# Kernel optimization log

Measured on AMD Instinct MI355X. Metric: run time of the kernel, lower is better.

## Reference

```python
import jax, jax.numpy as jnp
import numpy as np

NUM_EXPERT = 16
IN_FEAT = 1024
OUT_FEAT = 2048
N_TOKENS = 4096


def setup_inputs() -> dict:
    key = jax.random.key(0)
    k1, k2, k3 = jax.random.split(key, 3)
    x = jax.random.uniform(k1, (N_TOKENS, IN_FEAT), dtype=jnp.float32)
    gate = jax.random.randint(k2, (N_TOKENS,), 0, NUM_EXPERT, dtype=jnp.int32)
    # expert weights: [num_expert, out_feat, in_feat]
    weight = jax.random.normal(k3, (NUM_EXPERT, OUT_FEAT, IN_FEAT), dtype=jnp.float32) * 0.02
    return {"x": x, "gate": gate, "weight": weight}


def reference(x, gate, weight):
    # out[b] = weight[gate[b]] @ x[b]
    # Avoid materializing weight[gate] ([B, O, I] would be huge): scan over the
    # small, fixed expert axis with input masking (tokens not routed to expert e
    # contribute zero rows to that expert's GEMM).
    B = x.shape[0]
    E, O, I = weight.shape
    out0 = jnp.zeros((B, O), dtype=x.dtype)

    def body(out, ew):
        e, W = ew  # W: [O, I]
        xm = jnp.where((gate == e)[:, None], x, 0.0)  # [B, I] masked tokens
        return out + jnp.einsum("bi,oi->bo", xm, W), None

    out, _ = jax.lax.scan(body, out0, (jnp.arange(E), weight))
    return out
```

## Files before the change

kernel.cpp:

```cpp
#include <hip/hip_runtime.h>
#include <hip/hip_bf16.h>
#include <stdint.h>

#define N_TOKENS   4096
#define IN_FEAT    1024
#define OUT_FEAT   2048
#define NUM_EXPERT 16

#define BM 256
#define BN 128
#define BK 32
#define NT (IN_FEAT / BK)
#define MAX_TILES 32
#define MAX_ROWS  8192

typedef __bf16 bf16x8 __attribute__((ext_vector_type(8)));
typedef float  f32x4  __attribute__((ext_vector_type(4)));
typedef unsigned short us8 __attribute__((ext_vector_type(8)));

__device__ __forceinline__ unsigned short f32_to_bf16_rne(float f) {
  union { float f; uint32_t u; } v; v.f = f;
  uint32_t u = v.u;
  u += 0x7fffu + ((u >> 16) & 1u);
  return (unsigned short)(u >> 16);
}

__device__ __forceinline__ void async_copy16(const void* g, void* l) {
  __builtin_amdgcn_global_load_lds(
      (const __attribute__((address_space(1))) unsigned int*)g,
      (__attribute__((address_space(3))) unsigned int*)l, 16, 0, 0);
}

__global__ void k_setup(const int* __restrict__ gate,
                        int* __restrict__ pstart,
                        int* __restrict__ tile_e,
                        int* __restrict__ tile_m,
                        int* __restrict__ row_token)
{
  __shared__ int cnt[NUM_EXPERT];
  __shared__ int cur[NUM_EXPERT];
  __shared__ int ps[NUM_EXPERT];
  const int tid = threadIdx.x;
  if (tid < NUM_EXPERT) { cnt[tid] = 0; cur[tid] = 0; }
  __syncthreads();
  for (int b = tid; b < N_TOKENS; b += 256) atomicAdd(&cnt[gate[b]], 1);
  for (int r = tid; r < MAX_ROWS; r += 256) row_token[r] = -1;
  __syncthreads();
  if (tid == 0) {
    int p = 0, tot = 0;
    for (int e = 0; e < NUM_EXPERT; ++e) {
      ps[e] = p; pstart[e] = p;
      int nt = (cnt[e] + BM - 1) / BM;
      for (int t = 0; t < nt; ++t) { tile_e[tot] = e; tile_m[tot] = t; ++tot; }
      p += nt * BM;
    }
    for (int s = tot; s < MAX_TILES; ++s) { tile_e[s] = -1; tile_m[s] = 0; }
  }
  __syncthreads();
  for (int b = tid; b < N_TOKENS; b += 256) {
    int e = gate[b];
    int pos = atomicAdd(&cur[e], 1);
    row_token[ps[e] + pos] = b;
  }
}

__global__ void k_cast(const float4* __restrict__ x, us8* __restrict__ xs) {
  const int i = blockIdx.x * 256 + threadIdx.x;
  float4 a = x[i * 2];
  float4 b = x[i * 2 + 1];
  us8 o;
  o[0] = f32_to_bf16_rne(a.x); o[1] = f32_to_bf16_rne(a.y);
  o[2] = f32_to_bf16_rne(a.z); o[3] = f32_to_bf16_rne(a.w);
  o[4] = f32_to_bf16_rne(b.x); o[5] = f32_to_bf16_rne(b.y);
  o[6] = f32_to_bf16_rne(b.z); o[7] = f32_to_bf16_rne(b.w);
  xs[i] = o;
}

__global__ void __launch_bounds__(512, 4)
k_gemm(const unsigned short* __restrict__ xs,
       const float* __restrict__ w,
       const int* __restrict__ pstart,
       const int* __restrict__ tile_e,
       const int* __restrict__ tile_m,
       const int* __restrict__ row_token,
       float* __restrict__ out) {
  __shared__ us8   As[2][1024];
  __shared__ f32x4 Bs[2][1024];
  __shared__ int rowtok_s[BM];

  const int slot = blockIdx.y;
  const int e = tile_e[slot];
  if (e < 0) return;
  const int seg0 = pstart[e] + tile_m[slot] * BM;
  const int n0 = blockIdx.x * BN;

  const int tid  = threadIdx.x;
  const int wid  = tid >> 6;
  const int lane = tid & 63;
  const int lr   = lane & 15;
  const int quad = lane >> 4;
  const int wm   = (wid >> 1) * 64;
  const int wn   = (wid & 1) * 64;

  if (tid < BM) rowtok_s[tid] = row_token[seg0 + tid];

  const int cA = (tid & 3) ^ ((tid >> 3) & 3);
  const int rt0 = row_token[seg0 + (tid >> 2)];
  const int rt1 = row_token[seg0 + 128 + (tid >> 2)];
  const unsigned short* agp0 =
      xs + (size_t)(rt0 < 0 ? 0 : rt0) * IN_FEAT + cA * 8;
  const unsigned short* agp1 =
      xs + (size_t)(rt1 < 0 ? 0 : rt1) * IN_FEAT + cA * 8;

  const int cB = (tid & 7) ^ ((tid >> 3) & 7);
  const float* bgp = w + (size_t)e * OUT_FEAT * IN_FEAT
                       + (size_t)(n0 + (tid >> 3)) * IN_FEAT + cB * 4;

  f32x4 acc[4][4];
  const f32x4 z = {0.f, 0.f, 0.f, 0.f};
#pragma unroll
  for (int i = 0; i < 4; ++i)
#pragma unroll
    for (int j = 0; j < 4; ++j) acc[i][j] = z;

  auto stage = [&](int t, int b) {
    const int k0 = t * BK;
    async_copy16(agp0 + k0,                As[b] +       wid * 64);
    async_copy16(agp1 + k0,                As[b] + 512 + wid * 64);
    async_copy16(bgp + k0,                 Bs[b] +       wid * 64);
    async_copy16(bgp + 64 * IN_FEAT + k0,  Bs[b] + 512 + wid * 64);
  };

  stage(0, 0);

  asm volatile("s_waitcnt lgkmcnt(0)" ::: "memory");
  __builtin_amdgcn_s_barrier();

  for (int t = 0; t < NT; ++t) {
    const int buf = t & 1;
    if (t + 1 < NT) {
      stage(t + 1, buf ^ 1);
      asm volatile("s_waitcnt vmcnt(4)" ::: "memory");
    } else {
      asm volatile("s_waitcnt vmcnt(0)" ::: "memory");
    }
    __builtin_amdgcn_s_barrier();
    asm volatile("" ::: "memory");

    bf16x8 af[4], bf[4];
#pragma unroll
    for (int mi = 0; mi < 4; ++mi) {
      const int n = wm + mi * 16 + lr;
      af[mi] = *(const bf16x8*)&As[buf][n * 4 + (quad ^ ((n >> 1) & 3))];
    }
#pragma unroll
    for (int ni = 0; ni < 4; ++ni) {
      const int n = wn + ni * 16 + lr;
      f32x4 c0 = Bs[buf][n * 8 + ((2 * quad)     ^ (n & 7))];
      f32x4 c1 = Bs[buf][n * 8 + ((2 * quad + 1) ^ (n & 7))];
      bf16x8 b;
      b[0] = (__bf16)c0[0]; b[1] = (__bf16)c0[1];
      b[2] = (__bf16)c0[2]; b[3] = (__bf16)c0[3];
      b[4] = (__bf16)c1[0]; b[5] = (__bf16)c1[1];
      b[6] = (__bf16)c1[2]; b[7] = (__bf16)c1[3];
      bf[ni] = b;
    }
#pragma unroll
    for (int mi = 0; mi < 4; ++mi)
#pragma unroll
      for (int ni = 0; ni < 4; ++ni)
        acc[mi][ni] = __builtin_amdgcn_mfma_f32_16x16x32_bf16(
            af[mi], bf[ni], acc[mi][ni], 0, 0, 0);

    asm volatile("" ::: "memory");
    __builtin_amdgcn_s_barrier();
  }

#pragma unroll
  for (int mi = 0; mi < 4; ++mi) {
    const int mb = wm + mi * 16 + quad * 4;
    const int t0 = rowtok_s[mb + 0];
    const int t1 = rowtok_s[mb + 1];
    const int t2 = rowtok_s[mb + 2];
    const int t3 = rowtok_s[mb + 3];
#pragma unroll
    for (int ni = 0; ni < 4; ++ni) {
      const int n = n0 + wn + ni * 16 + lr;
      f32x4 c = acc[mi][ni];
      if (t0 >= 0) out[(size_t)t0 * OUT_FEAT + n] = c[0];
      if (t1 >= 0) out[(size_t)t1 * OUT_FEAT + n] = c[1];
      if (t2 >= 0) out[(size_t)t2 * OUT_FEAT + n] = c[2];
      if (t3 >= 0) out[(size_t)t3 * OUT_FEAT + n] = c[3];
    }
  }
}

extern "C" void kernel_launch(void* const* d_in, const int* in_sizes, int n_in,
                              void* d_out, int out_size, void* d_ws, size_t ws_size,
                              hipStream_t stream) {
  const float* x    = (const float*)d_in[0];
  const int*   gate = (const int*)d_in[1];
  const float* w    = (const float*)d_in[2];
  float* out = (float*)d_out;

  char* ws = (char*)d_ws;
  unsigned short* xs = (unsigned short*)ws;
  int* row_token = (int*)(ws + 8388608);
  int* pstart = row_token + MAX_ROWS;
  int* tile_e = pstart + NUM_EXPERT;
  int* tile_m = tile_e + MAX_TILES;

  k_setup<<<1, 256, 0, stream>>>(gate, pstart, tile_e, tile_m, row_token);
  k_cast<<<N_TOKENS * IN_FEAT / (8 * 256), 256, 0, stream>>>(
      (const float4*)x, (us8*)xs);
  dim3 g(OUT_FEAT / BN, MAX_TILES);
  k_gemm<<<g, 512, 0, stream>>>(xs, w, pstart, tile_e, tile_m, row_token, out);
}
```

Measured before the change: 264.9 us.

## Pre-cast expert weights to bf16 in a fused prep kernel, shrink GEMM tile to 128 rows

Adds a single prep kernel that does the routing setup and casts both x and all expert weights to bf16 in workspace. The GEMM then streams bf16 weights directly into LDS instead of fp32 with an in-loop conversion. The M tile shrinks to 128 with 256 threads and up to 48 tiles. If the workspace is too small it falls back to the old path. The cost is a full 128MB-read, 64MB-write weight cast on every call, which may outweigh halving the GEMM's weight traffic, plus more tiles each re-reading the weights.

```diff
diff --git a/kernel.cpp b/kernel.cpp
--- a/kernel.cpp
+++ b/kernel.cpp
@@ -7,12 +7,15 @@
 #define OUT_FEAT   2048
 #define NUM_EXPERT 16
 
-#define BM 256
+#define BM 128
 #define BN 128
 #define BK 32
 #define NT (IN_FEAT / BK)
-#define MAX_TILES 32
+#define MAX_TILES 48
 #define MAX_ROWS  8192
+
+#define XS_UNITS  (N_TOKENS * IN_FEAT / 8)
+#define WB_UNITS  (NUM_EXPERT * OUT_FEAT * IN_FEAT / 8)
 
 typedef __bf16 bf16x8 __attribute__((ext_vector_type(8)));
 typedef float  f32x4  __attribute__((ext_vector_type(4)));
@@ -31,12 +34,19 @@
       (__attribute__((address_space(3))) unsigned int*)l, 16, 0, 0);
 }
 
-__global__ void k_setup(const int* __restrict__ gate,
-                        int* __restrict__ pstart,
-                        int* __restrict__ tile_e,
-                        int* __restrict__ tile_m,
-                        int* __restrict__ row_token)
-{
+__device__ __forceinline__ us8 cast8(const float4 a, const float4 b) {
+  us8 o;
+  o[0] = f32_to_bf16_rne(a.x); o[1] = f32_to_bf16_rne(a.y);
+  o[2] = f32_to_bf16_rne(a.z); o[3] = f32_to_bf16_rne(a.w);
+  o[4] = f32_to_bf16_rne(b.x); o[5] = f32_to_bf16_rne(b.y);
+  o[6] = f32_to_bf16_rne(b.z); o[7] = f32_to_bf16_rne(b.w);
+  return o;
+}
+
+__device__ __forceinline__ void setup_body(
+    const int* __restrict__ gate, int* __restrict__ pstart,
+    int* __restrict__ tile_e, int* __restrict__ tile_m,
+    int* __restrict__ row_token, int qm, int max_tiles) {
   __shared__ int cnt[NUM_EXPERT];
   __shared__ int cur[NUM_EXPERT];
   __shared__ int ps[NUM_EXPERT];
@@ -50,11 +60,11 @@
     int p = 0, tot = 0;
     for (int e = 0; e < NUM_EXPERT; ++e) {
       ps[e] = p; pstart[e] = p;
-      int nt = (cnt[e] + BM - 1) / BM;
+      int nt = (cnt[e] + qm - 1) / qm;
       for (int t = 0; t < nt; ++t) { tile_e[tot] = e; tile_m[tot] = t; ++tot; }
-      p += nt * BM;
-    }
-    for (int s = tot; s < MAX_TILES; ++s) { tile_e[s] = -1; tile_m[s] = 0; }
+      p += nt * qm;
+    }
+    for (int s = tot; s < max_tiles; ++s) { tile_e[s] = -1; tile_m[s] = 0; }
   }
   __syncthreads();
   for (int b = tid; b < N_TOKENS; b += 256) {
@@ -64,28 +74,36 @@
   }
 }
 
-__global__ void k_cast(const float4* __restrict__ x, us8* __restrict__ xs) {
-  const int i = blockIdx.x * 256 + threadIdx.x;
-  float4 a = x[i * 2];
-  float4 b = x[i * 2 + 1];
-  us8 o;
-  o[0] = f32_to_bf16_rne(a.x); o[1] = f32_to_bf16_rne(a.y);
-  o[2] = f32_to_bf16_rne(a.z); o[3] = f32_to_bf16_rne(a.w);
-  o[4] = f32_to_bf16_rne(b.x); o[5] = f32_to_bf16_rne(b.y);
-  o[6] = f32_to_bf16_rne(b.z); o[7] = f32_to_bf16_rne(b.w);
-  xs[i] = o;
-}
-
-__global__ void __launch_bounds__(512, 4)
+__global__ void k_prep(const float4* __restrict__ x,
+                       const float4* __restrict__ w4,
+                       const int* __restrict__ gate,
+                       us8* __restrict__ xs, us8* __restrict__ wb,
+                       int* __restrict__ pstart, int* __restrict__ tile_e,
+                       int* __restrict__ tile_m, int* __restrict__ row_token) {
+  const int b = blockIdx.x;
+  if (b == 0) {
+    setup_body(gate, pstart, tile_e, tile_m, row_token, BM, MAX_TILES);
+    return;
+  }
+  const int i = (b - 1) * 256 + threadIdx.x;
+  if (i < XS_UNITS) {
+    xs[i] = cast8(x[i * 2], x[i * 2 + 1]);
+  } else {
+    const int j = i - XS_UNITS;
+    wb[j] = cast8(w4[j * 2], w4[j * 2 + 1]);
+  }
+}
+
+__global__ void __launch_bounds__(256)
 k_gemm(const unsigned short* __restrict__ xs,
-       const float* __restrict__ w,
+       const unsigned short* __restrict__ wb,
        const int* __restrict__ pstart,
        const int* __restrict__ tile_e,
        const int* __restrict__ tile_m,
        const int* __restrict__ row_token,
        float* __restrict__ out) {
-  __shared__ us8   As[2][1024];
-  __shared__ f32x4 Bs[2][1024];
+  __shared__ us8 As[2][512];
+  __shared__ us8 Bs[2][512];
   __shared__ int rowtok_s[BM];
 
   const int slot = blockIdx.y;
@@ -106,12 +124,131 @@
 
   const int cA = (tid & 3) ^ ((tid >> 3) & 3);
   const int rt0 = row_token[seg0 + (tid >> 2)];
-  const int rt1 = row_token[seg0 + 128 + (tid >> 2)];
+  const int rt1 = row_token[seg0 + 64 + (tid >> 2)];
   const unsigned short* agp0 =
       xs + (size_t)(rt0 < 0 ? 0 : rt0) * IN_FEAT + cA * 8;
   const unsigned short* agp1 =
       xs + (size_t)(rt1 < 0 ? 0 : rt1) * IN_FEAT + cA * 8;
-
+  const unsigned short* bgp =
+      wb + (size_t)e * OUT_FEAT * IN_FEAT
+         + (size_t)(n0 + (tid >> 2)) * IN_FEAT + cA * 8;
+
+  f32x4 acc[4][4];
+  const f32x4 z = {0.f, 0.f, 0.f, 0.f};
+#pragma unroll
+  for (int i = 0; i < 4; ++i)
+#pragma unroll
+    for (int j = 0; j < 4; ++j) acc[i][j] = z;
+
+  auto stage = [&](int t, int b) {
+    const int k0 = t * BK;
+    async_copy16(agp0 + k0,                As[b] +       wid * 64);
+    async_copy16(agp1 + k0,                As[b] + 256 + wid * 64);
+    async_copy16(bgp  + k0,                Bs[b] +       wid * 64);
+    async_copy16(bgp  + 64 * IN_FEAT + k0, Bs[b] + 256 + wid * 64);
+  };
+
+  stage(0, 0);
+
+  asm volatile("s_waitcnt lgkmcnt(0)" ::: "memory");
+  __builtin_amdgcn_s_barrier();
+
+  for (int t = 0; t < NT; ++t) {
+    const int buf = t & 1;
+    if (t + 1 < NT) {
+      stage(t + 1, buf ^ 1);
+      asm volatile("s_waitcnt vmcnt(4)" ::: "memory");
+    } else {
+      asm volatile("s_waitcnt vmcnt(0)" ::: "memory");
+    }
+    __builtin_amdgcn_s_barrier();
+    asm volatile("" ::: "memory");
+
+    bf16x8 af[4], bf[4];
+#pragma unroll
+    for (int mi = 0; mi < 4; ++mi) {
+      const int n = wm + mi * 16 + lr;
+      af[mi] = *(const bf16x8*)&As[buf][n * 4 + (quad ^ ((n >> 1) & 3))];
+    }
+#pragma unroll
+    for (int ni = 0; ni < 4; ++ni) {
+      const int n = wn + ni * 16 + lr;
+      bf[ni] = *(const bf16x8*)&Bs[buf][n * 4 + (quad ^ ((n >> 1) & 3))];
+    }
+#pragma unroll
+    for (int mi = 0; mi < 4; ++mi)
+#pragma unroll
+      for (int ni = 0; ni < 4; ++ni)
+        acc[mi][ni] = __builtin_amdgcn_mfma_f32_16x16x32_bf16(
+            af[mi], bf[ni], acc[mi][ni], 0, 0, 0);
+
+    asm volatile("" ::: "memory");
+    __builtin_amdgcn_s_barrier();
+  }
+
+#pragma unroll
+  for (int mi = 0; mi < 4; ++mi) {
+    const int mb = wm + mi * 16 + quad * 4;
+    const int t0 = rowtok_s[mb + 0];
+    const int t1 = rowtok_s[mb + 1];
+    const int t2 = rowtok_s[mb + 2];
+    const int t3 = rowtok_s[mb + 3];
+#pragma unroll
+    for (int ni = 0; ni < 4; ++ni) {
+      const int n = n0 + wn + ni * 16 + lr;
+      f32x4 c = acc[mi][ni];
+      if (t0 >= 0) out[(size_t)t0 * OUT_FEAT + n] = c[0];
+      if (t1 >= 0) out[(size_t)t1 * OUT_FEAT + n] = c[1];
+      if (t2 >= 0) out[(size_t)t2 * OUT_FEAT + n] = c[2];
+      if (t3 >= 0) out[(size_t)t3 * OUT_FEAT + n] = c[3];
+    }
+  }
+}
+
+__global__ void k_cast_v7(const float4* __restrict__ x, us8* __restrict__ xs) {
+  const int i = blockIdx.x * 256 + threadIdx.x;
+  xs[i] = cast8(x[i * 2], x[i * 2 + 1]);
+}
+
+__global__ void k_setup_v7(const int* __restrict__ gate, int* __restrict__ pstart,
+                           int* __restrict__ tile_e, int* __restrict__ tile_m,
+                           int* __restrict__ row_token) {
+  setup_body(gate, pstart, tile_e, tile_m, row_token, 256, 32);
+}
+
+__global__ void __launch_bounds__(512, 4)
+k_gemm_v7(const unsigned short* __restrict__ xs,
+          const float* __restrict__ w,
+          const int* __restrict__ pstart,
+          const int* __restrict__ tile_e,
+          const int* __restrict__ tile_m,
+          const int* __restrict__ row_token,
+          float* __restrict__ out) {
+  __shared__ us8   As[2][1024];
+  __shared__ f32x4 Bs[2][1024];
+  __shared__ int rowtok_s[256];
+
+  const int slot = blockIdx.y;
+  const int e = tile_e[slot];
+  if (e < 0) return;
+  const int seg0 = pstart[e] + tile_m[slot] * 256;
+  const int n0 = blockIdx.x * 128;
+
+  const int tid  = threadIdx.x;
+  const int wid  = tid >> 6;
+  const int lane = tid & 63;
+  const int lr   = lane & 15;
+  const int quad = lane >> 4;
+  const int wm   = (wid >> 1) * 64;
+  const int wn   = (wid & 1) * 64;
+
+  if (tid < 256) rowtok_s[tid] = row_token[seg0 + tid];
+
+  const int cA = (tid & 3) ^ ((tid >> 3) & 3);
+  const int rt0 = row_token[seg0 + (tid >> 2)];
+  const int rt1 = row_token[seg0 + 128 + (tid >> 2)];
+  const unsigned short* agp0 = xs + (size_t)(rt0 < 0 ? 0 : rt0) * IN_FEAT + cA * 8;
+  const unsigned short* agp1 = xs + (size_t)(rt1 < 0 ? 0 : rt1) * IN_FEAT + cA * 8;
   const int cB = (tid & 7) ^ ((tid >> 3) & 7);
   const float* bgp = w + (size_t)e * OUT_FEAT * IN_FEAT
                        + (size_t)(n0 + (tid >> 3)) * IN_FEAT + cB * 4;
@@ -132,7 +269,6 @@
   };
 
   stage(0, 0);
-
   asm volatile("s_waitcnt lgkmcnt(0)" ::: "memory");
   __builtin_amdgcn_s_barrier();
 
@@ -202,17 +338,37 @@
   const int*   gate = (const int*)d_in[1];
   const float* w    = (const float*)d_in[2];
   float* out = (float*)d_out;
-
   char* ws = (char*)d_ws;
-  unsigned short* xs = (unsigned short*)ws;
-  int* row_token = (int*)(ws + 8388608);
-  int* pstart = row_token + MAX_ROWS;
-  int* tile_e = pstart + NUM_EXPERT;
-  int* tile_m = tile_e + MAX_TILES;
-
-  k_setup<<<1, 256, 0, stream>>>(gate, pstart, tile_e, tile_m, row_token);
-  k_cast<<<N_TOKENS * IN_FEAT / (8 * 256), 256, 0, stream>>>(
-      (const float4*)x, (us8*)xs);
-  dim3 g(OUT_FEAT / BN, MAX_TILES);
-  k_gemm<<<g, 512, 0, stream>>>(xs, w, pstart, tile_e, tile_m, row_token, out);
-}
+
+  const size_t XS_B = 8u * 1024 * 1024;
+  const size_t WB_B = 64u * 1024 * 1024;
+  const size_t need = XS_B + WB_B + 64 * 1024;
+
+  if (ws_size >= need) {
+    unsigned short* xs = (unsigned short*)ws;
+    unsigned short* wb = (unsigned short*)(ws + XS_B);
+    int* row_token = (int*)(ws + XS_B + WB_B);
+    int* pstart = row_token + MAX_ROWS;
+    int* tile_e = pstart + NUM_EXPERT;
+    int* tile_m = tile_e + MAX_TILES;
+
+    k_prep<<<1 + (XS_UNITS + WB_UNITS) / 256, 256, 0, stream>>>(
+        (const float4*)x, (const float4*)w, gate,
+        (us8*)xs, (us8*)wb, pstart, tile_e, tile_m, row_token);
+    dim3 g(OUT_FEAT / BN, MAX_TILES);
+    k_gemm<<<g, 256, 0, stream>>>(xs, wb, pstart, tile_e, tile_m, row_token,
+                                  out);
+  } else {
+    unsigned short* xs = (unsigned short*)ws;
+    int* row_token = (int*)(ws + XS_B);
+    int* pstart = row_token + MAX_ROWS;
+    int* tile_e = pstart + NUM_EXPERT;
+    int* tile_m = tile_e + 32;
+
+    k_setup_v7<<<1, 256, 0, stream>>>(gate, pstart, tile_e, tile_m, row_token);
+    k_cast_v7<<<XS_UNITS / 256, 256, 0, stream>>>((const float4*)x, (us8*)xs);
+    dim3 g(OUT_FEAT / 128, 32);
+    k_gemm_v7<<<g, 512, 0, stream>>>(xs, w, pstart, tile_e, tile_m, row_token,
+                                     out);
+  }
+}
```

Measured after the change: 253.7 us. -4.2%, faster.
